# Kernel tuning notes

Hardware: AMD Instinct MI355X
Metric: run time of the kernel (lower is better)

Reference implementation:

```python
import jax, jax.numpy as jnp
import numpy as np

HID = 2048
HEADS = 16
HD = HID // HEADS  # 128


def setup_inputs() -> dict:
    key = jax.random.key(0)
    ks = jax.random.split(key, 9)
    s = 0.02
    return {
        "hidden_state": jax.random.normal(ks[0], (2, 2048, HID), dtype=jnp.float32),
        "Wq": jax.random.normal(ks[1], (HID, HID), dtype=jnp.float32) * s,
        "bq": jnp.zeros((HID,), dtype=jnp.float32),
        "Wk": jax.random.normal(ks[2], (HID, HD), dtype=jnp.float32) * s,
        "bk": jnp.zeros((HD,), dtype=jnp.float32),
        "Wv": jax.random.normal(ks[3], (HID, HD), dtype=jnp.float32) * s,
        "bv": jnp.zeros((HD,), dtype=jnp.float32),
        "Wo": jax.random.normal(ks[4], (HID, HID), dtype=jnp.float32) * s,
        "bo": jnp.zeros((HID,), dtype=jnp.float32),
    }


def reference(hidden_state, Wq, bq, Wk, bk, Wv, bv, Wo, bo):
    bs, seq, _ = hidden_state.shape
    # Q: [b, s, H, hd] -> per-head; K,V: single shared head [b, s, hd]
    q = (hidden_state @ Wq + bq).reshape(bs, seq, HEADS, HD)
    k = hidden_state @ Wk + bk  # [b, s, hd]
    v = hidden_state @ Wv + bv  # [b, s, hd]
    scale = 1.0 / jnp.sqrt(jnp.float32(HD))
    # scores: [b, h, s_q, s_k] against shared K head
    scores = jnp.einsum("bqhd,bkd->bhqk", q, k) * scale
    attn = jax.nn.softmax(scores, axis=-1)
    out = jnp.einsum("bhqk,bkd->bqhd", attn, v)  # [b, s, h, hd]
    out = out.reshape(bs, seq, HID)
    return out @ Wo + bo
```

## Files before the change

kernel.cpp:

```cpp
#include <hip/hip_runtime.h>
#include <math.h>

#define HIDN 2048
#define NHEADS 16
#define HDIM 128
#define SEQ 2048
#define NB 2

typedef __bf16 bf16x8 __attribute__((ext_vector_type(8)));
typedef float f32x4 __attribute__((ext_vector_type(4)));

__device__ __forceinline__ unsigned short f32_to_bf16(float f) {
  unsigned int u = __float_as_uint(f);
  u += 0x7FFFu + ((u >> 16) & 1u);
  return (unsigned short)(u >> 16);
}

__device__ __forceinline__ void gload_lds16(const void* g, void* l) {
  __builtin_amdgcn_global_load_lds(
      (__attribute__((address_space(1))) void*)(g),
      (__attribute__((address_space(3))) void*)(l), 16, 0, 0);
}

__global__ __launch_bounds__(256) void cast_f32_bf16(
    const float* __restrict__ in, unsigned short* __restrict__ out, int n4) {
  int i = blockIdx.x * blockDim.x + threadIdx.x;
  if (i >= n4) return;
  float4 v = ((const float4*)in)[i];
  ushort4 o;
  o.x = f32_to_bf16(v.x); o.y = f32_to_bf16(v.y);
  o.z = f32_to_bf16(v.z); o.w = f32_to_bf16(v.w);
  ((ushort4*)out)[i] = o;
}

__global__ __launch_bounds__(256) void wtrans_big(
    const float* __restrict__ wq, unsigned short* __restrict__ dq,
    const float* __restrict__ wo, unsigned short* __restrict__ do_) {
  __shared__ float tile[32][33];
  const float* src = blockIdx.z ? wo : wq;
  unsigned short* dst = blockIdx.z ? do_ : dq;
  int c0 = blockIdx.x * 32, r0 = blockIdx.y * 32;
  int tx = threadIdx.x & 31, ty = threadIdx.x >> 5;
#pragma unroll
  for (int i = 0; i < 32; i += 8)
    tile[ty + i][tx] = src[(size_t)(r0 + ty + i) * 2048 + c0 + tx];
  __syncthreads();
#pragma unroll
  for (int i = 0; i < 32; i += 8)
    dst[(size_t)(c0 + ty + i) * 2048 + r0 + tx] = f32_to_bf16(tile[tx][ty + i]);
}

__global__ __launch_bounds__(256) void wtrans_small(
    const float* __restrict__ wk, const float* __restrict__ wv,
    unsigned short* __restrict__ dk, unsigned short* __restrict__ dv,
    const float* __restrict__ bq, const float* __restrict__ bk,
    const float* __restrict__ bv, float* __restrict__ biasout) {
  __shared__ float tile[32][33];
  const float* src = blockIdx.z ? wv : wk;
  unsigned short* dst = blockIdx.z ? dv : dk;
  int c0 = blockIdx.x * 32, r0 = blockIdx.y * 32;
  int tx = threadIdx.x & 31, ty = threadIdx.x >> 5;
#pragma unroll
  for (int i = 0; i < 32; i += 8)
    tile[ty + i][tx] = src[(size_t)(r0 + ty + i) * 128 + c0 + tx];
  __syncthreads();
#pragma unroll
  for (int i = 0; i < 32; i += 8)
    dst[(size_t)(c0 + ty + i) * 2048 + r0 + tx] = f32_to_bf16(tile[tx][ty + i]);
  if (blockIdx.z == 0) {
    int lb = blockIdx.y * 4 + blockIdx.x;
    if (lb < 9) {
      int i = lb * 256 + threadIdx.x;
      if (i < 2304)
        biasout[i] = (i < 2048) ? bq[i] : ((i < 2176) ? bk[i - 2048] : bv[i - 2176]);
    }
  }
}

__global__ __launch_bounds__(256) void vtrans(
    const unsigned short* __restrict__ qkv, unsigned short* __restrict__ vt) {
  __shared__ unsigned short tile[32][33];
  const unsigned short* src = qkv + (size_t)blockIdx.z * SEQ * 2304 + 2176;
  unsigned short* dst = vt + (size_t)blockIdx.z * 128 * SEQ;
  int c0 = blockIdx.x * 32, r0 = blockIdx.y * 32;
  int tx = threadIdx.x & 31, ty = threadIdx.x >> 5;
#pragma unroll
  for (int i = 0; i < 32; i += 8)
    tile[ty + i][tx] = src[(size_t)(r0 + ty + i) * 2304 + c0 + tx];
  __syncthreads();
#pragma unroll
  for (int i = 0; i < 32; i += 8)
    dst[(size_t)(c0 + ty + i) * SEQ + r0 + tx] = tile[tx][ty + i];
}

template <int BN>
__global__ __launch_bounds__(256) void gemm_bt(
    const unsigned short* __restrict__ A,
    const unsigned short* __restrict__ BT,
    const float* __restrict__ bias,
    void* __restrict__ C, int K, int ldc, int outBf16) {
  constexpr int NT = BN / 32;
  __shared__ unsigned short As[128 * 64];
  __shared__ unsigned short Bs[BN * 64];
  const int tid = threadIdx.x;
  const int lane = tid & 63;
  const int wave = tid >> 6;
  const int wr = wave >> 1, wc = wave & 1;
  const int ml = lane & 15, quad = lane >> 4;
  const long bm = (long)blockIdx.x * 128;
  const long bn = (long)blockIdx.y * BN;

  const f32x4 zero4 = {0.f, 0.f, 0.f, 0.f};
  f32x4 acc[4][NT];
#pragma unroll
  for (int mt = 0; mt < 4; ++mt)
#pragma unroll
    for (int nt = 0; nt < NT; ++nt) acc[mt][nt] = zero4;

  const int srow = lane >> 3;
  const int scol = ((lane & 7) ^ srow) * 8;

  for (int k0 = 0; k0 < K; k0 += 64) {
    __syncthreads();
#pragma unroll
    for (int r = 0; r < 4; ++r) {
      const int rowb = r * 32 + wave * 8;
      gload_lds16(A + (bm + rowb + srow) * (long)K + k0 + scol, &As[rowb * 64]);
    }
#pragma unroll
    for (int r = 0; r < NT; ++r) {
      const int rowb = r * 32 + wave * 8;
      gload_lds16(BT + (bn + rowb + srow) * (long)K + k0 + scol, &Bs[rowb * 64]);
    }
    __syncthreads();
#pragma unroll
    for (int kk = 0; kk < 64; kk += 32) {
      const int g0 = (kk >> 3) + quad;
      bf16x8 af[4], bf[NT];
#pragma unroll
      for (int mt = 0; mt < 4; ++mt)
        af[mt] = *(const bf16x8*)&As[(wr * 64 + mt * 16 + ml) * 64 +
                                     ((g0 ^ (ml & 7)) << 3)];
#pragma unroll
      for (int nt = 0; nt < NT; ++nt)
        bf[nt] = *(const bf16x8*)&Bs[(wc * (BN / 2) + nt * 16 + ml) * 64 +
                                     ((g0 ^ (ml & 7)) << 3)];
#pragma unroll
      for (int mt = 0; mt < 4; ++mt)
#pragma unroll
        for (int nt = 0; nt < NT; ++nt)
          acc[mt][nt] = __builtin_amdgcn_mfma_f32_16x16x32_bf16(
              af[mt], bf[nt], acc[mt][nt], 0, 0, 0);
    }
  }

#pragma unroll
  for (int mt = 0; mt < 4; ++mt) {
#pragma unroll
    for (int nt = 0; nt < NT; ++nt) {
      const long col = bn + wc * (BN / 2) + nt * 16 + ml;
      const float bval = bias ? bias[col] : 0.f;
#pragma unroll
      for (int r = 0; r < 4; ++r) {
        const long row = bm + wr * 64 + mt * 16 + quad * 4 + r;
        const float v = acc[mt][nt][r] + bval;
        if (outBf16)
          ((unsigned short*)C)[row * ldc + col] = f32_to_bf16(v);
        else
          ((float*)C)[row * ldc + col] = v;
      }
    }
  }
}

__global__ __launch_bounds__(256, 4) void mqa_attn(
    const unsigned short* __restrict__ qkv,
    const unsigned short* __restrict__ vt,
    unsigned short* __restrict__ outp) {
  __shared__ unsigned short Ks[64 * 128];
  __shared__ unsigned short VTs[128 * 64];
  __shared__ unsigned short Ps[64 * 64];

  const int tid = threadIdx.x;
  const int lane = tid & 63;
  const int wave = tid >> 6;
  const int ml = lane & 15, quad = lane >> 4;
  const int qt = blockIdx.x, h = blockIdx.y, b = blockIdx.z;
  const long q0 = (long)qt * 64;
  const long base = (long)b * SEQ;

  bf16x8 aq[4];
  {
    const unsigned short* qrow = qkv + (base + q0 + wave * 16 + ml) * 2304 + h * 128;
#pragma unroll
    for (int ks = 0; ks < 4; ++ks)
      aq[ks] = *(const bf16x8*)(qrow + ks * 32 + quad * 8);
  }

  const f32x4 zero4 = {0.f, 0.f, 0.f, 0.f};
  f32x4 o_acc[8];
#pragma unroll
  for (int nt = 0; nt < 8; ++nt) o_acc[nt] = zero4;
  float l_i[4] = {0.f, 0.f, 0.f, 0.f};
  const float c2 = 0.08838834764831845f * 1.4426950408889634f;

  const int srowK = lane >> 4;
  const int scolK = ((lane & 15) ^ (wave * 4 + srowK)) * 8;
  const int srowV = lane >> 3;
  const int scolV = ((lane & 7) ^ srowV) * 8;
  const unsigned short* kp = qkv + (base + srowK) * 2304 + 2048 + scolK;
  const unsigned short* vp = vt + ((long)b * 128 + srowV) * SEQ + scolV;

  for (int kt = 0; kt < SEQ / 64; ++kt) {
    __syncthreads();
#pragma unroll
    for (int r = 0; r < 4; ++r) {
      const int rowb = r * 16 + wave * 4;
      gload_lds16(kp + (long)rowb * 2304, &Ks[rowb * 128]);
    }
#pragma unroll
    for (int r = 0; r < 4; ++r) {
      const int rowb = r * 32 + wave * 8;
      gload_lds16(vp + (long)rowb * SEQ, &VTs[rowb * 64]);
    }
    kp += 64 * 2304;
    vp += 64;
    __syncthreads();

    f32x4 s[4];
#pragma unroll
    for (int nt = 0; nt < 4; ++nt) s[nt] = zero4;
#pragma unroll
    for (int ks = 0; ks < 4; ++ks) {
      const int g0 = ks * 4 + quad;
#pragma unroll
      for (int nt = 0; nt < 4; ++nt) {
        bf16x8 bk8 = *(const bf16x8*)&Ks[(nt * 16 + ml) * 128 + ((g0 ^ ml) << 3)];
        s[nt] = __builtin_amdgcn_mfma_f32_16x16x32_bf16(aq[ks], bk8, s[nt], 0, 0, 0);
      }
    }

#pragma unroll
    for (int nt = 0; nt < 4; ++nt)
#pragma unroll
      for (int r = 0; r < 4; ++r) {
        const float p = exp2f(s[nt][r] * c2);
        l_i[r] += p;
        const int pr = wave * 16 + quad * 4 + r;
        const int g = nt * 2 + (ml >> 3);
        Ps[pr * 64 + (((g ^ (pr & 7)) << 3) | (ml & 7))] = f32_to_bf16(p);
      }

#pragma unroll
    for (int ks = 0; ks < 2; ++ks) {
      const int g0 = ks * 4 + quad;
      bf16x8 ap = *(const bf16x8*)&Ps[(wave * 16 + ml) * 64 + ((g0 ^ (ml & 7)) << 3)];
#pragma unroll
      for (int nt = 0; nt < 8; ++nt) {
        bf16x8 bv8 = *(const bf16x8*)&VTs[(nt * 16 + ml) * 64 + ((g0 ^ (ml & 7)) << 3)];
        o_acc[nt] = __builtin_amdgcn_mfma_f32_16x16x32_bf16(ap, bv8, o_acc[nt], 0, 0, 0);
      }
    }
  }

  float inv_l[4];
#pragma unroll
  for (int r = 0; r < 4; ++r) {
    float rs = l_i[r];
#pragma unroll
    for (int off = 1; off < 16; off <<= 1) rs += __shfl_xor(rs, off);
    inv_l[r] = 1.f / rs;
  }
#pragma unroll
  for (int nt = 0; nt < 8; ++nt)
#pragma unroll
    for (int r = 0; r < 4; ++r) {
      const long row = base + q0 + wave * 16 + quad * 4 + r;
      outp[row * HIDN + h * HDIM + nt * 16 + ml] =
          f32_to_bf16(o_acc[nt][r] * inv_l[r]);
    }
}

extern "C" void kernel_launch(void* const* d_in, const int* in_sizes, int n_in,
                              void* d_out, int out_size, void* d_ws, size_t ws_size,
                              hipStream_t stream) {
  const float* hidden = (const float*)d_in[0];
  const float* Wq = (const float*)d_in[1];
  const float* bq = (const float*)d_in[2];
  const float* Wk = (const float*)d_in[3];
  const float* bk = (const float*)d_in[4];
  const float* Wv = (const float*)d_in[5];
  const float* bv = (const float*)d_in[6];
  const float* Wo = (const float*)d_in[7];
  const float* bo = (const float*)d_in[8];
  float* out = (float*)d_out;

  char* ws = (char*)d_ws;
  const size_t MB = 1u << 20;
  unsigned short* hb    = (unsigned short*)(ws);
  unsigned short* attn  = hb;
  unsigned short* wqkvT = (unsigned short*)(ws + 16 * MB);
  unsigned short* woT   = (unsigned short*)(ws + 25 * MB);
  unsigned short* qkv   = (unsigned short*)(ws + 33 * MB);
  unsigned short* vt    = (unsigned short*)(ws + 51 * MB);
  float* biasqkv        = (float*)(ws + 52 * MB);

  cast_f32_bf16<<<8192, 256, 0, stream>>>(hidden, hb, (NB * SEQ * HIDN) / 4);
  wtrans_big<<<dim3(64, 64, 2), 256, 0, stream>>>(Wq, wqkvT, Wo, woT);
  wtrans_small<<<dim3(4, 64, 2), 256, 0, stream>>>(
      Wk, Wv, wqkvT + (size_t)2048 * 2048, wqkvT + (size_t)2176 * 2048,
      bq, bk, bv, biasqkv);

  gemm_bt<96><<<dim3(32, 24), 256, 0, stream>>>(hb, wqkvT, biasqkv, qkv, 2048, 2304, 1);

  vtrans<<<dim3(4, 64, 2), 256, 0, stream>>>(qkv, vt);

  mqa_attn<<<dim3(SEQ / 64, NHEADS, NB), 256, 0, stream>>>(qkv, vt, attn);

  gemm_bt<128><<<dim3(32, 16), 256, 0, stream>>>(attn, woT, bo, out, 2048, 2048, 0);
}
```

Baseline: 323.1 us.

## Restructure MQA attention: transposed scores, register P, double-buffered K/V, 128-row tiles

The attention kernel now computes the transposed score tile (K as the A operand, Q as B), so P stays in registers and feeds the PV MFMA directly. This removes the LDS round trip through Ps. To make that register layout line up, the V transpose kernel permutes columns within each 64-wide block. K/V tiles are double-buffered so the next tile's global-to-LDS load overlaps compute, and each block handles 128 query rows instead of 64, doubling K/V reuse. The cost is more registers and lower occupancy (launch bound 2 instead of 4) and an extra layout coupling between vtrans and the attention kernel.

```diff
diff --git a/kernel.cpp b/kernel.cpp
--- a/kernel.cpp
+++ b/kernel.cpp
@@ -14,6 +14,10 @@
   unsigned int u = __float_as_uint(f);
   u += 0x7FFFu + ((u >> 16) & 1u);
   return (unsigned short)(u >> 16);
+}
+
+__device__ __forceinline__ unsigned pack_bf16x2(float a, float b) {
+  return (unsigned)f32_to_bf16(a) | ((unsigned)f32_to_bf16(b) << 16);
 }
 
 __device__ __forceinline__ void gload_lds16(const void* g, void* l) {
@@ -88,9 +92,12 @@
   for (int i = 0; i < 32; i += 8)
     tile[ty + i][tx] = src[(size_t)(r0 + ty + i) * 2304 + c0 + tx];
   __syncthreads();
-#pragma unroll
-  for (int i = 0; i < 32; i += 8)
-    dst[(size_t)(c0 + ty + i) * SEQ + r0 + tx] = tile[tx][ty + i];
+  const int s = r0 + tx;
+  const int col = (s & ~63) | (((s >> 5) & 1) * 32 + ((s >> 2) & 3) * 8 +
+                               ((s >> 4) & 1) * 4 + (s & 3));
+#pragma unroll
+  for (int i = 0; i < 32; i += 8)
+    dst[(size_t)(c0 + ty + i) * SEQ + col] = tile[tx][ty + i];
 }
 
 template <int BN>
@@ -173,35 +180,37 @@
   }
 }
 
-__global__ __launch_bounds__(256, 4) void mqa_attn(
+__global__ __launch_bounds__(256, 2) void mqa_attn(
     const unsigned short* __restrict__ qkv,
     const unsigned short* __restrict__ vt,
     unsigned short* __restrict__ outp) {
-  __shared__ unsigned short Ks[64 * 128];
-  __shared__ unsigned short VTs[128 * 64];
-  __shared__ unsigned short Ps[64 * 64];
-
-  const int tid = threadIdx.x;
-  const int lane = tid & 63;
-  const int wave = tid >> 6;
+  __shared__ unsigned short Ks[2][64 * 128];
+  __shared__ unsigned short VTs[2][128 * 64];
+
+  const int lane = threadIdx.x & 63;
+  const int wave = threadIdx.x >> 6;
   const int ml = lane & 15, quad = lane >> 4;
-  const int qt = blockIdx.x, h = blockIdx.y, b = blockIdx.z;
-  const long q0 = (long)qt * 64;
+  const int h = blockIdx.y, b = blockIdx.z;
+  const long q0 = (long)blockIdx.x * 128;
   const long base = (long)b * SEQ;
 
-  bf16x8 aq[4];
-  {
-    const unsigned short* qrow = qkv + (base + q0 + wave * 16 + ml) * 2304 + h * 128;
+  bf16x8 aq[2][4];
+#pragma unroll
+  for (int n = 0; n < 2; ++n) {
+    const unsigned short* qrow =
+        qkv + (base + q0 + wave * 32 + n * 16 + ml) * 2304 + h * 128;
 #pragma unroll
     for (int ks = 0; ks < 4; ++ks)
-      aq[ks] = *(const bf16x8*)(qrow + ks * 32 + quad * 8);
+      aq[n][ks] = *(const bf16x8*)(qrow + ks * 32 + quad * 8);
   }
 
   const f32x4 zero4 = {0.f, 0.f, 0.f, 0.f};
-  f32x4 o_acc[8];
-#pragma unroll
-  for (int nt = 0; nt < 8; ++nt) o_acc[nt] = zero4;
-  float l_i[4] = {0.f, 0.f, 0.f, 0.f};
+  f32x4 o[8][2];
+#pragma unroll
+  for (int mt2 = 0; mt2 < 8; ++mt2)
+#pragma unroll
+    for (int n = 0; n < 2; ++n) o[mt2][n] = zero4;
+  float l[2] = {0.f, 0.f};
   const float c2 = 0.08838834764831845f * 1.4426950408889634f;
 
   const int srowK = lane >> 4;
@@ -211,74 +220,103 @@
   const unsigned short* kp = qkv + (base + srowK) * 2304 + 2048 + scolK;
   const unsigned short* vp = vt + ((long)b * 128 + srowV) * SEQ + scolV;
 
-  for (int kt = 0; kt < SEQ / 64; ++kt) {
-    __syncthreads();
+  auto stage = [&](int buf, int ktn) {
+    const unsigned short* kpp = kp + (long)ktn * (64 * 2304);
+    const unsigned short* vpp = vp + ktn * 64;
 #pragma unroll
     for (int r = 0; r < 4; ++r) {
       const int rowb = r * 16 + wave * 4;
-      gload_lds16(kp + (long)rowb * 2304, &Ks[rowb * 128]);
+      gload_lds16(kpp + (long)rowb * 2304, &Ks[buf][rowb * 128]);
     }
 #pragma unroll
     for (int r = 0; r < 4; ++r) {
       const int rowb = r * 32 + wave * 8;
-      gload_lds16(vp + (long)rowb * SEQ, &VTs[rowb * 64]);
-    }
-    kp += 64 * 2304;
-    vp += 64;
+      gload_lds16(vpp + (long)rowb * SEQ, &VTs[buf][rowb * 64]);
+    }
+  };
+
+  stage(0, 0);
+
+  for (int kt = 0; kt < SEQ / 64; ++kt) {
+    const int cur = kt & 1;
     __syncthreads();
-
-    f32x4 s[4];
-#pragma unroll
-    for (int nt = 0; nt < 4; ++nt) s[nt] = zero4;
+    if (kt < SEQ / 64 - 1) stage(cur ^ 1, kt + 1);
+
+    f32x4 s[4][2];
+#pragma unroll
+    for (int mt = 0; mt < 4; ++mt)
+#pragma unroll
+      for (int n = 0; n < 2; ++n) s[mt][n] = zero4;
 #pragma unroll
     for (int ks = 0; ks < 4; ++ks) {
-      const int g0 = ks * 4 + quad;
-#pragma unroll
-      for (int nt = 0; nt < 4; ++nt) {
-        bf16x8 bk8 = *(const bf16x8*)&Ks[(nt * 16 + ml) * 128 + ((g0 ^ ml) << 3)];
-        s[nt] = __builtin_amdgcn_mfma_f32_16x16x32_bf16(aq[ks], bk8, s[nt], 0, 0, 0);
-      }
-    }
-
-#pragma unroll
-    for (int nt = 0; nt < 4; ++nt)
-#pragma unroll
-      for (int r = 0; r < 4; ++r) {
-        const float p = exp2f(s[nt][r] * c2);
-        l_i[r] += p;
-        const int pr = wave * 16 + quad * 4 + r;
-        const int g = nt * 2 + (ml >> 3);
-        Ps[pr * 64 + (((g ^ (pr & 7)) << 3) | (ml & 7))] = f32_to_bf16(p);
-      }
-
-#pragma unroll
-    for (int ks = 0; ks < 2; ++ks) {
-      const int g0 = ks * 4 + quad;
-      bf16x8 ap = *(const bf16x8*)&Ps[(wave * 16 + ml) * 64 + ((g0 ^ (ml & 7)) << 3)];
-#pragma unroll
-      for (int nt = 0; nt < 8; ++nt) {
-        bf16x8 bv8 = *(const bf16x8*)&VTs[(nt * 16 + ml) * 64 + ((g0 ^ (ml & 7)) << 3)];
-        o_acc[nt] = __builtin_amdgcn_mfma_f32_16x16x32_bf16(ap, bv8, o_acc[nt], 0, 0, 0);
-      }
-    }
-  }
-
-  float inv_l[4];
-#pragma unroll
-  for (int r = 0; r < 4; ++r) {
-    float rs = l_i[r];
-#pragma unroll
-    for (int off = 1; off < 16; off <<= 1) rs += __shfl_xor(rs, off);
-    inv_l[r] = 1.f / rs;
-  }
-#pragma unroll
-  for (int nt = 0; nt < 8; ++nt)
-#pragma unroll
-    for (int r = 0; r < 4; ++r) {
-      const long row = base + q0 + wave * 16 + quad * 4 + r;
-      outp[row * HIDN + h * HDIM + nt * 16 + ml] =
-          f32_to_bf16(o_acc[nt][r] * inv_l[r]);
-    }
+#pragma unroll
+      for (int mt = 0; mt < 4; ++mt) {
+        bf16x8 ak = *(const bf16x8*)&Ks[cur][(mt * 16 + ml) * 128 +
+                                            (((ks * 4 + quad) ^ ml) << 3)];
+#pragma unroll
+        for (int n = 0; n < 2; ++n)
+          s[mt][n] = __builtin_amdgcn_mfma_f32_16x16x32_bf16(
+              ak, aq[n][ks], s[mt][n], 0, 0, 0);
+      }
+    }
+
+    unsigned pk[2][4][2];
+#pragma unroll
+    for (int mt = 0; mt < 4; ++mt)
+#pragma unroll
+      for (int n = 0; n < 2; ++n) {
+        const float p0 = exp2f(s[mt][n][0] * c2);
+        const float p1 = exp2f(s[mt][n][1] * c2);
+        const float p2 = exp2f(s[mt][n][2] * c2);
+        const float p3 = exp2f(s[mt][n][3] * c2);
+        l[n] += (p0 + p1) + (p2 + p3);
+        pk[n][mt][0] = pack_bf16x2(p0, p1);
+        pk[n][mt][1] = pack_bf16x2(p2, p3);
+      }
+
+#pragma unroll
+    for (int ks2 = 0; ks2 < 2; ++ks2) {
+      bf16x8 bp[2];
+#pragma unroll
+      for (int n = 0; n < 2; ++n) {
+        union { unsigned u[4]; bf16x8 v; } cv;
+        cv.u[0] = pk[n][2 * ks2][0];
+        cv.u[1] = pk[n][2 * ks2][1];
+        cv.u[2] = pk[n][2 * ks2 + 1][0];
+        cv.u[3] = pk[n][2 * ks2 + 1][1];
+        bp[n] = cv.v;
+      }
+#pragma unroll
+      for (int mt2 = 0; mt2 < 8; ++mt2) {
+        bf16x8 av = *(const bf16x8*)&VTs[cur][(mt2 * 16 + ml) * 64 +
+                                             (((ks2 * 4 + quad) ^ (ml & 7)) << 3)];
+#pragma unroll
+        for (int n = 0; n < 2; ++n)
+          o[mt2][n] = __builtin_amdgcn_mfma_f32_16x16x32_bf16(
+              av, bp[n], o[mt2][n], 0, 0, 0);
+      }
+    }
+  }
+
+  float inv[2];
+#pragma unroll
+  for (int n = 0; n < 2; ++n) {
+    float rs = l[n];
+    rs += __shfl_xor(rs, 16);
+    rs += __shfl_xor(rs, 32);
+    inv[n] = 1.f / rs;
+  }
+#pragma unroll
+  for (int n = 0; n < 2; ++n) {
+    const long row = base + q0 + wave * 32 + n * 16 + ml;
+#pragma unroll
+    for (int mt2 = 0; mt2 < 8; ++mt2) {
+      uint2 w;
+      w.x = pack_bf16x2(o[mt2][n][0] * inv[n], o[mt2][n][1] * inv[n]);
+      w.y = pack_bf16x2(o[mt2][n][2] * inv[n], o[mt2][n][3] * inv[n]);
+      *(uint2*)&outp[row * HIDN + h * HDIM + mt2 * 16 + quad * 4] = w;
+    }
+  }
 }
 
 extern "C" void kernel_launch(void* const* d_in, const int* in_sizes, int n_in,
@@ -315,7 +353,7 @@
 
   vtrans<<<dim3(4, 64, 2), 256, 0, stream>>>(qkv, vt);
 
-  mqa_attn<<<dim3(SEQ / 64, NHEADS, NB), 256, 0, stream>>>(qkv, vt, attn);
+  mqa_attn<<<dim3(SEQ / 128, NHEADS, NB), 256, 0, stream>>>(qkv, vt, attn);
 
   gemm_bt<128><<<dim3(32, 16), 256, 0, stream>>>(attn, woT, bo, out, 2048, 2048, 0);
 }
```

Result: no change. 317.9 us (-1.6%).
